# Kernel tuning notes

Measured on AMD Instinct MI355X. Metric: run time of the kernel, lower is better.

The kernel has to match this reference:

```python
import jax, jax.numpy as jnp
import numpy as np

G, N, K, H, D = 16, 256, 128, 32, 768
NUM_ATOM_TYPES = 128
NUM_EDGE_TYPES = NUM_ATOM_TYPES * NUM_ATOM_TYPES  # 16384
T_STEPS = 1000


def setup_inputs() -> dict:
    key = jax.random.key(0)
    ks = jax.random.split(key, 12)
    return {
        "pos": jax.random.normal(ks[0], (G, N, 3), dtype=jnp.float32) * 3.0,
        "x": jax.random.randint(ks[1], (G, N, 1), 0, NUM_ATOM_TYPES, dtype=jnp.int32),
        "t": jax.random.randint(ks[2], (G,), 0, T_STEPS, dtype=jnp.int32),
        "means": jax.random.uniform(ks[3], (T_STEPS, K), jnp.float32, 0.0, 3.0),
        "stds": jax.random.uniform(ks[4], (T_STEPS, K), jnp.float32, 0.0, 3.0),
        "mul_w": jnp.ones((NUM_EDGE_TYPES, 1), jnp.float32),
        "bias_w": jnp.zeros((NUM_EDGE_TYPES, 1), jnp.float32),
        "w1": jax.random.normal(ks[5], (K, K), jnp.float32) / np.sqrt(K),
        "b1": jnp.zeros((K,), jnp.float32),
        "w2": jax.random.normal(ks[6], (K, H), jnp.float32) / np.sqrt(K),
        "b2": jnp.zeros((H,), jnp.float32),
        "we": jax.random.normal(ks[7], (K, D), jnp.float32) / np.sqrt(K),
        "be": jnp.zeros((D,), jnp.float32),
    }


def _forward(pos, x, t, means, stds, mul_w, bias_w, w1, b1, w2, b2, we, be):
    atoms = x[:, :, 0]  # [G, N]
    edge_types = atoms[:, :, None] * NUM_ATOM_TYPES + atoms[:, None, :]  # [G,N,N]
    pad = atoms == 0  # [G, N]
    pos = jnp.where(pad[..., None], 0.0, pos)
    # delta_pos[g,i,j] = pos[g,j] - pos[g,i]
    delta_pos = pos[:, None, :, :] - pos[:, :, None, :]  # [G,N,N,3]
    sq = jnp.sum(delta_pos * delta_pos, axis=-1)  # [G,N,N]
    dist = jnp.sqrt(jnp.where(sq > 0, sq, 1.0)) * (sq > 0)  # safe norm, grad-safe at 0
    delta_pos = delta_pos / (dist[..., None] + 1e-5)
    # Gaussian basis expansion
    mul = mul_w[edge_types]   # [G,N,N,1]
    bias = bias_w[edge_types]  # [G,N,N,1]
    xg = mul * dist[..., None] + bias  # [G,N,N,1] -> broadcasts to K
    mean = means[t][:, None, None, :]               # [G,1,1,K]
    std = jnp.abs(stds[t])[:, None, None, :] + 1e-5  # [G,1,1,K]
    a = (2.0 * 3.14159) ** 0.5
    z = (xg - mean) / std
    edge_feature = jnp.exp(-0.5 * z * z) / (a * std)  # [G,N,N,K]
    # NonLinear MLP -> attn bias per head
    h = jax.nn.gelu(edge_feature @ w1 + b1, approximate=False)
    attn_bias = h @ w2 + b2  # [G,N,N,H]
    attn_bias = jnp.transpose(attn_bias, (0, 3, 1, 2))  # [G,H,N,N]
    attn_bias = jnp.where(pad[:, None, None, :], -jnp.inf, attn_bias)
    # masked sum over source nodes + edge projection
    ef = jnp.where(pad[:, None, :, None], 0.0, edge_feature)
    sum_ef = jnp.sum(ef, axis=-2)  # [G,N,K]
    merge = sum_ef @ we + be  # [G,N,D]
    return dist, delta_pos, attn_bias, merge


def reference(pos, x, t, means, stds, mul_w, bias_w, w1, b1, w2, b2, we, be):
    return _forward(pos, x, t, means, stds, mul_w, bias_w, w1, b1, w2, b2, we, be)
```

## Files before the change

### kernel.cpp

```cpp
#include <hip/hip_runtime.h>
#include <hip/hip_bf16.h>
#include <math.h>

#define Gn 16
#define Nn 256
#define Kf 128
#define Hh 32
#define Dd 768
#define NEG_BIG (-3.0e38f)
#define PAD_XG  (1.0e10f)
#define INV_A 0.3989422804014327f
#define NHALF_LOG2E (-0.7213475204444817f)
#define HSIG_A 0.2837f

typedef __attribute__((ext_vector_type(8))) short bf16x8;
typedef __attribute__((ext_vector_type(4))) float f32x4;

static __device__ __forceinline__ float fast_exp2(float x) {
#if __has_builtin(__builtin_amdgcn_exp2f)
    return __builtin_amdgcn_exp2f(x);
#else
    return exp2f(x);
#endif
}
static __device__ __forceinline__ float clamp01(float x) {
#if __has_builtin(__builtin_amdgcn_fmed3f)
    return __builtin_amdgcn_fmed3f(x, 0.f, 1.f);
#else
    return fminf(fmaxf(x, 0.f), 1.f);
#endif
}

static __device__ __forceinline__ unsigned short f2bf(float f) {
    union { float f; unsigned int u; } v; v.f = f;
    unsigned int r = v.u + 0x7FFF + ((v.u >> 16) & 1);
    return (unsigned short)(r >> 16);
}

__global__ __launch_bounds__(256)
void prep_kernel(const float* __restrict__ w1, const float* __restrict__ w2,
                 const int* __restrict__ tarr, const float* __restrict__ means,
                 const float* __restrict__ stds,
                 unsigned short* __restrict__ w1f, unsigned short* __restrict__ w2f,
                 float4* __restrict__ coef)
{
    const int idx = blockIdx.x * 256 + threadIdx.x;
    if (idx < 2048) {
        const int lane = idx & 63;
        const int nf   = (idx >> 6) & 7;
        const int ks   = idx >> 9;
        const int l15 = lane & 15, lhi = lane >> 4;
        const int n = nf * 16 + l15;
        unsigned short v[8];
#pragma unroll
        for (int e = 0; e < 8; ++e) {
            const int k = ks * 32 + lhi * 8 + e;
            v[e] = f2bf(w1[k * Kf + n]);
        }
        *(uint4*)(w1f + (size_t)idx * 8) = *(const uint4*)v;
    } else if (idx < 2560) {
        const int f2 = idx - 2048;
        const int lane = f2 & 63;
        const int mf   = (f2 >> 6) & 1;
        const int ks   = f2 >> 7;
        const int l15 = lane & 15, lhi = lane >> 4;
        const int m = mf * 16 + l15;
        unsigned short v[8];
#pragma unroll
        for (int e = 0; e < 8; ++e) {
            const int k = ks * 32 + lhi * 8 + e;
            v[e] = f2bf(w2[k * Hh + m]);
        }
        *(uint4*)(w2f + (size_t)f2 * 8) = *(const uint4*)v;
    } else if (idx < 4608) {
        const int e3 = idx - 2560;
        const int g = e3 >> 7, k = e3 & 127;
        const int tg = tarr[g];
        const float mean = means[tg * Kf + k];
        const float sd   = fabsf(stds[tg * Kf + k]) + 1e-5f;
        const float inv  = 1.0f / sd;
        coef[g * Kf + k] =
            make_float4(mean, NHALF_LOG2E * inv * inv, log2f(inv * INV_A), 0.f);
    }
}

__global__ __launch_bounds__(256, 4)
void graph3d_attn_kernel(const float* __restrict__ pos,
                         const int* __restrict__ atoms,
                         const float* __restrict__ mul_w,
                         const float* __restrict__ bias_w,
                         const float* __restrict__ b1,
                         const float* __restrict__ b2,
                         const unsigned short* __restrict__ w1f,
                         const unsigned short* __restrict__ w2f,
                         const float4* __restrict__ coef,
                         float* __restrict__ ws_sum,
                         float* __restrict__ out_dist,
                         float* __restrict__ out_delta,
                         float* __restrict__ out_attn)
{
    const int tid  = threadIdx.x;
    const int half = blockIdx.x;
    const int i    = blockIdx.y;
    const int g    = blockIdx.z;
    const int j0   = half * 128;

    __shared__ __align__(16) unsigned short s_tile[128 * 128];

    const int lane = tid & 63, wq = tid >> 6;
    const int l15 = lane & 15, lhi = lane >> 4;

    if (lane < 32) {
        const int ai = atoms[g * Nn + i];
        float pix = pos[(g * Nn + i) * 3 + 0];
        float piy = pos[(g * Nn + i) * 3 + 1];
        float piz = pos[(g * Nn + i) * 3 + 2];
        if (ai == 0) { pix = 0.f; piy = 0.f; piz = 0.f; }

        const int j  = j0 + wq * 32 + lane;
        const int aj = atoms[g * Nn + j];
        float pjx = pos[(g * Nn + j) * 3 + 0];
        float pjy = pos[(g * Nn + j) * 3 + 1];
        float pjz = pos[(g * Nn + j) * 3 + 2];
        if (aj == 0) { pjx = 0.f; pjy = 0.f; pjz = 0.f; }
        const float dx = pjx - pix, dy = pjy - piy, dz = pjz - piz;
        const float sq = dx * dx + dy * dy + dz * dz;
        const float dist = (sq > 0.f) ? sqrtf(sq) : 0.f;
        const float inv_d = 1.f / (dist + 1e-5f);
        const size_t base = (size_t)(g * Nn + i) * Nn + j;
        out_dist[base] = dist;
        out_delta[base * 3 + 0] = dx * inv_d;
        out_delta[base * 3 + 1] = dy * inv_d;
        out_delta[base * 3 + 2] = dz * inv_d;
        const int et = ai * 128 + aj;
        float xg = fmaf(mul_w[et], dist, bias_w[et]);
        if (aj == 0) xg = PAD_XG;
        ((float*)((char*)s_tile + (size_t)(wq * 32 + 31) * 256))[lane] = xg;
    }

    const int kq = lane & 31;
    f32x4 ps = (f32x4){0.f, 0.f, 0.f, 0.f};
    {
        const int jh = lane >> 5;
        const float4 c0 = coef[g * Kf + 4 * kq + 0];
        const float4 c1 = coef[g * Kf + 4 * kq + 1];
        const float4 c2 = coef[g * Kf + 4 * kq + 2];
        const float4 c3 = coef[g * Kf + 4 * kq + 3];
        char* rowbase = (char*)s_tile + wq * 32 * 256;
        const float* xgp = (const float*)((char*)s_tile + (wq * 32 + 31) * 256)
                           + jh * 16;
        const int colb = 8 * kq;
#pragma unroll
        for (int q4 = 0; q4 < 4; ++q4) {
            const float4 x4 = *(const float4*)(xgp + q4 * 4);
#pragma unroll
            for (int u = 0; u < 4; ++u) {
                const int j = jh * 16 + q4 * 4 + u;
                const float x = ((const float*)&x4)[u];
                const float d0 = x - c0.x, d1 = x - c1.x;
                const float d2 = x - c2.x, d3 = x - c3.x;
                const float e0 = fast_exp2(fmaf(c0.y, d0 * d0, c0.z));
                const float e1 = fast_exp2(fmaf(c1.y, d1 * d1, c1.z));
                const float e2 = fast_exp2(fmaf(c2.y, d2 * d2, c2.z));
                const float e3 = fast_exp2(fmaf(c3.y, d3 * d3, c3.z));
                ps += (f32x4){e0, e1, e2, e3};
                const __hip_bfloat162 p0 = __float22bfloat162_rn(make_float2(e0, e1));
                const __hip_bfloat162 p1 = __float22bfloat162_rn(make_float2(e2, e3));
                uint2 u2;
                u2.x = *(const unsigned int*)&p0;
                u2.y = *(const unsigned int*)&p1;
                *(uint2*)(rowbase + j * 256 + (colb ^ ((j & 7) << 4))) = u2;
            }
        }
        ps.x += __shfl_xor(ps.x, 32);
        ps.y += __shfl_xor(ps.y, 32);
        ps.z += __shfl_xor(ps.z, 32);
        ps.w += __shfl_xor(ps.w, 32);
    }

    const int jrow0 = wq * 32 + l15, jrow1 = jrow0 + 16;
    char* tb0 = (char*)s_tile + jrow0 * 256;
    char* tb1 = (char*)s_tile + jrow1 * 256;
    const int sw0 = (jrow0 & 7) << 4, sw1 = (jrow1 & 7) << 4;
    const unsigned short* w1p = w1f + lane * 8;
    const unsigned short* w2p = w2f + lane * 8;

    f32x4 acc[8][2];
#pragma unroll
    for (int a = 0; a < 8; ++a)
#pragma unroll
        for (int b = 0; b < 2; ++b) acc[a][b] = (f32x4){0.f, 0.f, 0.f, 0.f};

#pragma unroll
    for (int ks = 0; ks < 4; ++ks) {
        const int kb = ks * 64 + lhi * 16;
        const bf16x8 b0  = *(const bf16x8*)(tb0 + (kb ^ sw0));
        const bf16x8 b1f = *(const bf16x8*)(tb1 + (kb ^ sw1));
        bf16x8 a0[4];
#pragma unroll
        for (int nf = 0; nf < 4; ++nf)
            a0[nf] = *(const bf16x8*)(w1p + (ks * 8 + nf) * 512);
#pragma unroll
        for (int nf = 0; nf < 4; ++nf) {
            acc[nf][0] = __builtin_amdgcn_mfma_f32_16x16x32_bf16(a0[nf], b0,  acc[nf][0], 0, 0, 0);
            acc[nf][1] = __builtin_amdgcn_mfma_f32_16x16x32_bf16(a0[nf], b1f, acc[nf][1], 0, 0, 0);
        }
        bf16x8 a1[4];
#pragma unroll
        for (int nf = 0; nf < 4; ++nf)
            a1[nf] = *(const bf16x8*)(w1p + (ks * 8 + nf + 4) * 512);
#pragma unroll
        for (int nf = 0; nf < 4; ++nf) {
            acc[nf + 4][0] = __builtin_amdgcn_mfma_f32_16x16x32_bf16(a1[nf], b0,  acc[nf + 4][0], 0, 0, 0);
            acc[nf + 4][1] = __builtin_amdgcn_mfma_f32_16x16x32_bf16(a1[nf], b1f, acc[nf + 4][1], 0, 0, 0);
        }
    }

#pragma unroll
    for (int nf = 0; nf < 8; ++nf) {
        const float4 bbv = *(const float4*)(b1 + nf * 16 + lhi * 4);
        const f32x4 bb = (f32x4){bbv.x, bbv.y, bbv.z, bbv.w};
        const int colb = 32 * nf + 8 * lhi;
#pragma unroll
        for (int jf = 0; jf < 2; ++jf) {
            char* tb = jf ? tb1 : tb0;
            const int sw = jf ? sw1 : sw0;
            const f32x4 v = acc[nf][jf] + bb;
            f32x4 h;
#pragma unroll
            for (int r = 0; r < 4; ++r)
                h[r] = v[r] * clamp01(fmaf(HSIG_A, v[r], 0.5f));
            const __hip_bfloat162 p0 = __float22bfloat162_rn(make_float2(h.x, h.y));
            const __hip_bfloat162 p1 = __float22bfloat162_rn(make_float2(h.z, h.w));
            uint2 u;
            u.x = *(const unsigned int*)&p0;
            u.y = *(const unsigned int*)&p1;
            *(uint2*)(tb + (colb ^ sw)) = u;
        }
    }

    f32x4 acc2[2][2];
#pragma unroll
    for (int a = 0; a < 2; ++a)
#pragma unroll
        for (int b = 0; b < 2; ++b) acc2[a][b] = (f32x4){0.f, 0.f, 0.f, 0.f};

#pragma unroll
    for (int ks = 0; ks < 4; ++ks) {
        const int kb = ks * 64 + lhi * 16;
        const bf16x8 bh0 = *(const bf16x8*)(tb0 + (kb ^ sw0));
        const bf16x8 bh1 = *(const bf16x8*)(tb1 + (kb ^ sw1));
#pragma unroll
        for (int mf = 0; mf < 2; ++mf) {
            const bf16x8 a2 = *(const bf16x8*)(w2p + (ks * 2 + mf) * 512);
            acc2[mf][0] = __builtin_amdgcn_mfma_f32_16x16x32_bf16(a2, bh0, acc2[mf][0], 0, 0, 0);
            acc2[mf][1] = __builtin_amdgcn_mfma_f32_16x16x32_bf16(a2, bh1, acc2[mf][1], 0, 0, 0);
        }
    }

    const size_t attn_g = (size_t)g * Hh * (Nn * Nn) + (size_t)i * Nn + j0;
    const float4 b2lo = *(const float4*)(b2 + lhi * 4);
    const float4 b2hi = *(const float4*)(b2 + 16 + lhi * 4);
#pragma unroll
    for (int jf = 0; jf < 2; ++jf) {
        const int jloc = wq * 32 + jf * 16 + l15;
        const bool keep = atoms[g * Nn + j0 + jloc] != 0;
#pragma unroll
        for (int mf = 0; mf < 2; ++mf) {
            const float4 b2v = mf ? b2hi : b2lo;
            const f32x4 v = acc2[mf][jf] + (f32x4){b2v.x, b2v.y, b2v.z, b2v.w};
#pragma unroll
            for (int r = 0; r < 4; ++r) {
                const int m = mf * 16 + lhi * 4 + r;
                out_attn[attn_g + (size_t)m * (Nn * Nn) + jloc] =
                    keep ? v[r] : NEG_BIG;
            }
        }
    }

    __syncthreads();
    if (lane < 32) {
        float* pt = (float*)s_tile;
        *(f32x4*)&pt[wq * 128 + 4 * kq] = ps;
    }
    __syncthreads();
    if (tid < 128) {
        const float* pt = (const float*)s_tile;
        const float s = (pt[tid] + pt[128 + tid]) + (pt[256 + tid] + pt[384 + tid]);
        ws_sum[((size_t)(g * Nn + i) * 2 + half) * Kf + tid] = s;
    }
}

__global__ __launch_bounds__(256)
void graph3d_merge_kernel(const float* __restrict__ ws_sum,
                          const float* __restrict__ we,
                          const float* __restrict__ be,
                          float* __restrict__ out_merge)
{
    const int tid = threadIdx.x;
    const int bd  = blockIdx.x;
    const int r0  = blockIdx.y * 16;
    __shared__ __align__(16) float s_rows[16][128];

#pragma unroll
    for (int p = 0; p < 8; ++p) {
        const int e = p * 256 + tid;
        const int r = e >> 7, k = e & 127;
        const size_t gi = (size_t)(r0 + r);
        s_rows[r][k] = ws_sum[(gi * 2 + 0) * Kf + k] + ws_sum[(gi * 2 + 1) * Kf + k];
    }
    __syncthreads();

    const int col = bd * 256 + tid;
    float acc[16];
#pragma unroll
    for (int r = 0; r < 16; ++r) acc[r] = 0.f;

    for (int k4 = 0; k4 < 32; ++k4) {
        const int k = k4 * 4;
        const float w0  = we[(k + 0) * Dd + col];
        const float w1v = we[(k + 1) * Dd + col];
        const float w2v = we[(k + 2) * Dd + col];
        const float w3  = we[(k + 3) * Dd + col];
#pragma unroll
        for (int r = 0; r < 16; ++r) {
            const float4 s = ((const float4*)&s_rows[r][0])[k4];
            acc[r] = fmaf(s.x, w0, acc[r]);
            acc[r] = fmaf(s.y, w1v, acc[r]);
            acc[r] = fmaf(s.z, w2v, acc[r]);
            acc[r] = fmaf(s.w, w3, acc[r]);
        }
    }

    const float b = be[col];
#pragma unroll
    for (int r = 0; r < 16; ++r)
        out_merge[(size_t)(r0 + r) * Dd + col] = acc[r] + b;
}

extern "C" void kernel_launch(void* const* d_in, const int* in_sizes, int n_in,
                              void* d_out, int out_size, void* d_ws, size_t ws_size,
                              hipStream_t stream) {
    const float* pos    = (const float*)d_in[0];
    const int*   x      = (const int*)  d_in[1];
    const int*   t      = (const int*)  d_in[2];
    const float* means  = (const float*)d_in[3];
    const float* stds   = (const float*)d_in[4];
    const float* mul_w  = (const float*)d_in[5];
    const float* bias_w = (const float*)d_in[6];
    const float* w1     = (const float*)d_in[7];
    const float* b1     = (const float*)d_in[8];
    const float* w2     = (const float*)d_in[9];
    const float* b2     = (const float*)d_in[10];
    const float* we     = (const float*)d_in[11];
    const float* be     = (const float*)d_in[12];

    float* out = (float*)d_out;
    float* out_dist  = out;
    float* out_delta = out + (size_t)Gn * Nn * Nn;
    float* out_attn  = out + (size_t)Gn * Nn * Nn * 4;
    float* out_merge = out + (size_t)Gn * Nn * Nn * 4 + (size_t)Gn * Hh * Nn * Nn;

    float* ws_sum = (float*)d_ws;
    unsigned short* w1f = (unsigned short*)((char*)d_ws + (size_t)Gn * Nn * 2 * Kf * 4);
    unsigned short* w2f = w1f + 2048 * 8;
    float4* coef = (float4*)(w2f + 512 * 8);

    prep_kernel<<<18, 256, 0, stream>>>(w1, w2, t, means, stds, w1f, w2f, coef);

    dim3 gridA(2, Nn, Gn);
    graph3d_attn_kernel<<<gridA, 256, 0, stream>>>(
        pos, x, mul_w, bias_w, b1, b2, w1f, w2f, coef,
        ws_sum, out_dist, out_delta, out_attn);

    dim3 gridB(3, 256);
    graph3d_merge_kernel<<<gridB, 256, 0, stream>>>(
        ws_sum, we, be, out_merge);
}
```

Baseline: 112.8 us.

## Split pairwise geometry into a separate kernel feeding an xg table

Moves distance, unit-vector and Gaussian-input computation out of the main attention kernel into a new geometry kernel that writes dist, delta and an xg table to workspace. The attention kernel then reads xg from global memory instead of computing it in a divergent prologue staged through shared memory. This removes per-block prologue work and the divergent lanes, at the cost of an extra launch and a 4 MB xg table round trip through memory. It also drops the shared-memory sync dependency on the prologue.

```diff
diff --git a/kernel.cpp b/kernel.cpp
--- a/kernel.cpp
+++ b/kernel.cpp
@@ -84,19 +84,58 @@
     }
 }
 
+__global__ __launch_bounds__(256)
+void geom_kernel(const float* __restrict__ pos,
+                 const int* __restrict__ atoms,
+                 const float* __restrict__ mul_w,
+                 const float* __restrict__ bias_w,
+                 float* __restrict__ xg_tab,
+                 float* __restrict__ out_dist,
+                 float* __restrict__ out_delta)
+{
+    const int j  = threadIdx.x;
+    const int i0 = blockIdx.x * 4;
+    const int g  = blockIdx.y;
+
+    const int aj = atoms[g * Nn + j];
+    float pjx = pos[(g * Nn + j) * 3 + 0];
+    float pjy = pos[(g * Nn + j) * 3 + 1];
+    float pjz = pos[(g * Nn + j) * 3 + 2];
+    if (aj == 0) { pjx = 0.f; pjy = 0.f; pjz = 0.f; }
+
+#pragma unroll
+    for (int ii = 0; ii < 4; ++ii) {
+        const int iv = i0 + ii;
+        const int ai = atoms[g * Nn + iv];
+        float pix = pos[(g * Nn + iv) * 3 + 0];
+        float piy = pos[(g * Nn + iv) * 3 + 1];
+        float piz = pos[(g * Nn + iv) * 3 + 2];
+        if (ai == 0) { pix = 0.f; piy = 0.f; piz = 0.f; }
+        const float dx = pjx - pix, dy = pjy - piy, dz = pjz - piz;
+        const float sq = dx * dx + dy * dy + dz * dz;
+        const float dist = (sq > 0.f) ? sqrtf(sq) : 0.f;
+        const float inv_d = 1.f / (dist + 1e-5f);
+        const size_t base = (size_t)(g * Nn + iv) * Nn + j;
+        out_dist[base] = dist;
+        out_delta[base * 3 + 0] = dx * inv_d;
+        out_delta[base * 3 + 1] = dy * inv_d;
+        out_delta[base * 3 + 2] = dz * inv_d;
+        const int et = ai * 128 + aj;
+        float xg = fmaf(mul_w[et], dist, bias_w[et]);
+        if (aj == 0) xg = PAD_XG;
+        xg_tab[base] = xg;
+    }
+}
+
 __global__ __launch_bounds__(256, 4)
-void graph3d_attn_kernel(const float* __restrict__ pos,
-                         const int* __restrict__ atoms,
-                         const float* __restrict__ mul_w,
-                         const float* __restrict__ bias_w,
+void graph3d_attn_kernel(const int* __restrict__ atoms,
                          const float* __restrict__ b1,
                          const float* __restrict__ b2,
                          const unsigned short* __restrict__ w1f,
                          const unsigned short* __restrict__ w2f,
                          const float4* __restrict__ coef,
+                         const float* __restrict__ xg_tab,
                          float* __restrict__ ws_sum,
-                         float* __restrict__ out_dist,
-                         float* __restrict__ out_delta,
                          float* __restrict__ out_attn)
 {
     const int tid  = threadIdx.x;
@@ -109,34 +148,6 @@
 
     const int lane = tid & 63, wq = tid >> 6;
     const int l15 = lane & 15, lhi = lane >> 4;
-
-    if (lane < 32) {
-        const int ai = atoms[g * Nn + i];
-        float pix = pos[(g * Nn + i) * 3 + 0];
-        float piy = pos[(g * Nn + i) * 3 + 1];
-        float piz = pos[(g * Nn + i) * 3 + 2];
-        if (ai == 0) { pix = 0.f; piy = 0.f; piz = 0.f; }
-
-        const int j  = j0 + wq * 32 + lane;
-        const int aj = atoms[g * Nn + j];
-        float pjx = pos[(g * Nn + j) * 3 + 0];
-        float pjy = pos[(g * Nn + j) * 3 + 1];
-        float pjz = pos[(g * Nn + j) * 3 + 2];
-        if (aj == 0) { pjx = 0.f; pjy = 0.f; pjz = 0.f; }
-        const float dx = pjx - pix, dy = pjy - piy, dz = pjz - piz;
-        const float sq = dx * dx + dy * dy + dz * dz;
-        const float dist = (sq > 0.f) ? sqrtf(sq) : 0.f;
-        const float inv_d = 1.f / (dist + 1e-5f);
-        const size_t base = (size_t)(g * Nn + i) * Nn + j;
-        out_dist[base] = dist;
-        out_delta[base * 3 + 0] = dx * inv_d;
-        out_delta[base * 3 + 1] = dy * inv_d;
-        out_delta[base * 3 + 2] = dz * inv_d;
-        const int et = ai * 128 + aj;
-        float xg = fmaf(mul_w[et], dist, bias_w[et]);
-        if (aj == 0) xg = PAD_XG;
-        ((float*)((char*)s_tile + (size_t)(wq * 32 + 31) * 256))[lane] = xg;
-    }
 
     const int kq = lane & 31;
     f32x4 ps = (f32x4){0.f, 0.f, 0.f, 0.f};
@@ -147,7 +158,7 @@
         const float4 c2 = coef[g * Kf + 4 * kq + 2];
         const float4 c3 = coef[g * Kf + 4 * kq + 3];
         char* rowbase = (char*)s_tile + wq * 32 * 256;
-        const float* xgp = (const float*)((char*)s_tile + (wq * 32 + 31) * 256)
+        const float* xgp = xg_tab + (size_t)(g * Nn + i) * Nn + j0 + wq * 32
                            + jh * 16;
         const int colb = 8 * kq;
 #pragma unroll
@@ -362,16 +373,20 @@
     float* out_merge = out + (size_t)Gn * Nn * Nn * 4 + (size_t)Gn * Hh * Nn * Nn;
 
     float* ws_sum = (float*)d_ws;
-    unsigned short* w1f = (unsigned short*)((char*)d_ws + (size_t)Gn * Nn * 2 * Kf * 4);
+    float* xg_tab = ws_sum + (size_t)Gn * Nn * 2 * Kf;
+    unsigned short* w1f = (unsigned short*)(xg_tab + (size_t)Gn * Nn * Nn);
     unsigned short* w2f = w1f + 2048 * 8;
     float4* coef = (float4*)(w2f + 512 * 8);
 
     prep_kernel<<<18, 256, 0, stream>>>(w1, w2, t, means, stds, w1f, w2f, coef);
 
+    dim3 gridG(Nn / 4, Gn);
+    geom_kernel<<<gridG, 256, 0, stream>>>(pos, x, mul_w, bias_w,
+                                           xg_tab, out_dist, out_delta);
+
     dim3 gridA(2, Nn, Gn);
     graph3d_attn_kernel<<<gridA, 256, 0, stream>>>(
-        pos, x, mul_w, bias_w, b1, b2, w1f, w2f, coef,
-        ws_sum, out_dist, out_delta, out_attn);
+        x, b1, b2, w1f, w2f, coef, xg_tab, ws_sum, out_attn);
 
     dim3 gridB(3, 256);
     graph3d_merge_kernel<<<gridB, 256, 0, stream>>>(
```

After: 122.6 us. 8.7% more time.
